# Kernel optimization log

Measured on AMD Instinct MI355X. Metric: run time of the kernel, lower is better.

## Reference

```python
import jax, jax.numpy as jnp
import numpy as np

H, W, K = 256, 256, 512
Z_THRESHOLD = 3.0
EPS = 1e-8


def setup_inputs() -> dict:
    key = jax.random.key(0)
    k1, k2, k3, k4 = jax.random.split(key, 4)
    # positions uniform in [0,H] x [0,W] x [0,64]
    positions = jax.random.uniform(k1, (K, 3)) * jnp.array([H, W, 64.0], jnp.float32)
    # scales: sigma_x, sigma_y in [1,5]; sigma_z in [0.5,2]
    s_xy = 1.0 + 4.0 * jax.random.uniform(k2, (K, 2))
    s_z = 0.5 + 1.5 * jax.random.uniform(k2, (K, 1))
    scales = jnp.concatenate([s_xy, s_z], axis=-1)
    opacity = jax.random.uniform(k3, (K,))
    intensity = jax.random.uniform(k4, (K,))
    z_target = jnp.array([32.0], jnp.float32)
    return {"positions": positions, "scales": scales, "opacity": opacity,
            "intensity": intensity, "z_target": z_target}


def reference(positions, scales, opacity, intensity, z_target):
    # z culling: instead of boolean gather (data-dependent shape), zero out
    # effective weights of culled Gaussians -> identical math (alpha=0 terms
    # contribute nothing and leave transmittance unchanged).
    z_dist = (z_target - positions[:, 2]) / (scales[:, 2] + EPS)          # (K,)
    z_mask = jnp.abs(z_dist) < Z_THRESHOLD
    z_weight = jnp.exp(-0.5 * z_dist ** 2)
    eff_w = jnp.where(z_mask, opacity * z_weight, 0.0)                    # (K,)

    grid_y = jnp.arange(H, dtype=positions.dtype)[:, None, None]         # (H,1,1)
    grid_x = jnp.arange(W, dtype=positions.dtype)[None, :, None]         # (1,W,1)
    # matches torch: dx pairs row-coord with mu_x, dy pairs col-coord with mu_y
    dxn = (grid_y - positions[:, 0]) / (scales[:, 0] + EPS)               # (H,W,K)
    dyn = (grid_x - positions[:, 1]) / (scales[:, 1] + EPS)               # (H,W,K)
    gauss = jnp.exp(-0.5 * (dxn ** 2 + dyn ** 2))                         # (H,W,K)

    # alpha compositing, sorted by weight descending
    alpha = jnp.clip(gauss * eff_w, 0.0, 0.99)
    order = jnp.argsort(-eff_w)
    alpha = alpha[:, :, order]
    s_int = intensity[order]
    trans = jnp.cumprod(1.0 - alpha, axis=-1)
    trans = jnp.concatenate([jnp.ones_like(trans[:, :, :1]), trans[:, :, :-1]], axis=-1)
    rendered = jnp.sum(trans * alpha * s_int, axis=-1)                    # (H,W)
    return rendered[None]                                                 # (1,H,W)
```

## Files before the change

### kernel.cpp

```cpp
#include <hip/hip_runtime.h>

#define IH 256
#define IW 256
#define NK 512
#define ZTH 3.0f
#define EPSV 1e-8f

__launch_bounds__(256, 4)
__global__ void slice_render_fused(const float* __restrict__ positions,
                                   const float* __restrict__ scales,
                                   const float* __restrict__ opacity,
                                   const float* __restrict__ intensity,
                                   const float* __restrict__ z_target,
                                   float* __restrict__ out) {
    __shared__ float s_pos[3 * NK];
    __shared__ float s_scl[3 * NK];
    __shared__ float s_opa[NK];
    __shared__ float s_int[NK];
    __shared__ float s_w[NK];
    __shared__ int   s_idx[NK];
    __shared__ float s_py[NK], s_isy[NK], s_rowfac[NK], s_it[NK];
    __shared__ int   s_cnt;

    const int tid = threadIdx.x;
    const float zt = z_target[0];

    for (int i = tid; i < 3 * NK; i += 256) {
        s_pos[i] = positions[i];
        s_scl[i] = scales[i];
    }
    for (int i = tid; i < NK; i += 256) {
        s_opa[i] = opacity[i];
        s_int[i] = intensity[i];
    }
    if (tid == 0) s_cnt = 0;
    __syncthreads();

    for (int k = tid; k < NK; k += 256) {
        float zd = (zt - s_pos[3 * k + 2]) / (s_scl[3 * k + 2] + EPSV);
        float w = 0.0f;
        if (fabsf(zd) < ZTH) w = s_opa[k] * __expf(-0.5f * zd * zd);
        if (w > 0.0f) {
            int p = atomicAdd(&s_cnt, 1);
            s_w[p] = w;
            s_idx[p] = k;
        }
    }
    __syncthreads();

    const int m = s_cnt;
    if (m == 0) { out[blockIdx.x * IW + tid] = 0.0f; return; }

    int msort = 2;
    while (msort < m) msort <<= 1;

    for (int k = m + tid; k < msort; k += 256) { s_w[k] = -1.0f; s_idx[k] = NK; }

    const int half = msort >> 1;
    for (int size = 2; size <= msort; size <<= 1) {
        for (int stride = size >> 1; stride > 0; stride >>= 1) {
            __syncthreads();
            for (int p = tid; p < half; p += 256) {
                int i = ((p & ~(stride - 1)) << 1) | (p & (stride - 1));
                int j = i | stride;
                bool desc = ((i & size) == 0);
                float wi = s_w[i], wj = s_w[j];
                int   ii = s_idx[i], ij = s_idx[j];
                bool cb_ji = (wj > wi) || (wj == wi && ij < ii);
                bool cb_ij = (wi > wj) || (wi == wj && ii < ij);
                if (desc ? cb_ji : cb_ij) {
                    s_w[i] = wj;  s_w[j] = wi;
                    s_idx[i] = ij; s_idx[j] = ii;
                }
            }
        }
    }
    __syncthreads();

    const float y = (float)blockIdx.x;
    for (int k = tid; k < m; k += 256) {
        int j = s_idx[k];
        float px  = s_pos[3 * j + 0];
        float isx = 1.0f / (s_scl[3 * j + 0] + EPSV);
        float dx  = (y - px) * isx;
        s_rowfac[k] = __expf(-0.5f * dx * dx) * s_w[k];
        s_py[k]   = s_pos[3 * j + 1];
        s_isy[k]  = 1.0f / (s_scl[3 * j + 1] + EPSV);
        s_it[k]   = s_int[j];
    }
    __syncthreads();

    const float x = (float)tid;
    float T = 1.0f;
    float acc = 0.0f;
    for (int k = 0; k < m; ++k) {
        float dy = (x - s_py[k]) * s_isy[k];
        float a  = fminf(__expf(-0.5f * dy * dy) * s_rowfac[k], 0.99f);
        acc += T * a * s_it[k];
        T   *= 1.0f - a;
        if (__all(T < 1e-6f)) break;
    }
    out[blockIdx.x * IW + tid] = acc;
}

extern "C" void kernel_launch(void* const* d_in, const int* in_sizes, int n_in,
                              void* d_out, int out_size, void* d_ws, size_t ws_size,
                              hipStream_t stream) {
    (void)in_sizes; (void)n_in; (void)out_size; (void)d_ws; (void)ws_size;
    const float* positions = (const float*)d_in[0];
    const float* scales    = (const float*)d_in[1];
    const float* opacity   = (const float*)d_in[2];
    const float* intensity = (const float*)d_in[3];
    const float* z_target  = (const float*)d_in[4];
    float* out = (float*)d_out;
    hipLaunchKernelGGL(slice_render_fused, dim3(IH), dim3(256), 0, stream,
                       positions, scales, opacity, intensity, z_target, out);
}
```

Baseline: 76.54 us.

## Replace bitonic sort with rank sort and pack per-gaussian data into float4

After: 69.65 us. 9.0% less time.

```diff
diff --git a/kernel.cpp b/kernel.cpp
--- a/kernel.cpp
+++ b/kernel.cpp
@@ -13,33 +13,21 @@
                                    const float* __restrict__ intensity,
                                    const float* __restrict__ z_target,
                                    float* __restrict__ out) {
-    __shared__ float s_pos[3 * NK];
-    __shared__ float s_scl[3 * NK];
-    __shared__ float s_opa[NK];
-    __shared__ float s_int[NK];
-    __shared__ float s_w[NK];
-    __shared__ int   s_idx[NK];
-    __shared__ float s_py[NK], s_isy[NK], s_rowfac[NK], s_it[NK];
-    __shared__ int   s_cnt;
+    __shared__ float  s_w[NK];
+    __shared__ int    s_idx[NK];
+    __shared__ float4 s_srt[NK + 8];
+    __shared__ int    s_cnt;
 
     const int tid = threadIdx.x;
     const float zt = z_target[0];
 
-    for (int i = tid; i < 3 * NK; i += 256) {
-        s_pos[i] = positions[i];
-        s_scl[i] = scales[i];
-    }
-    for (int i = tid; i < NK; i += 256) {
-        s_opa[i] = opacity[i];
-        s_int[i] = intensity[i];
-    }
     if (tid == 0) s_cnt = 0;
     __syncthreads();
 
     for (int k = tid; k < NK; k += 256) {
-        float zd = (zt - s_pos[3 * k + 2]) / (s_scl[3 * k + 2] + EPSV);
+        float zd = (zt - positions[3 * k + 2]) / (scales[3 * k + 2] + EPSV);
         float w = 0.0f;
-        if (fabsf(zd) < ZTH) w = s_opa[k] * __expf(-0.5f * zd * zd);
+        if (fabsf(zd) < ZTH) w = opacity[k] * __expf(-0.5f * zd * zd);
         if (w > 0.0f) {
             int p = atomicAdd(&s_cnt, 1);
             s_w[p] = w;
@@ -48,56 +36,44 @@
     }
     __syncthreads();
 
-    const int m = s_cnt;
-    if (m == 0) { out[blockIdx.x * IW + tid] = 0.0f; return; }
+    const int m  = s_cnt;
+    const int mp = (m + 7) & ~7;
+    const float y = (float)blockIdx.x;
 
-    int msort = 2;
-    while (msort < m) msort <<= 1;
-
-    for (int k = m + tid; k < msort; k += 256) { s_w[k] = -1.0f; s_idx[k] = NK; }
-
-    const int half = msort >> 1;
-    for (int size = 2; size <= msort; size <<= 1) {
-        for (int stride = size >> 1; stride > 0; stride >>= 1) {
-            __syncthreads();
-            for (int p = tid; p < half; p += 256) {
-                int i = ((p & ~(stride - 1)) << 1) | (p & (stride - 1));
-                int j = i | stride;
-                bool desc = ((i & size) == 0);
-                float wi = s_w[i], wj = s_w[j];
-                int   ii = s_idx[i], ij = s_idx[j];
-                bool cb_ji = (wj > wi) || (wj == wi && ij < ii);
-                bool cb_ij = (wi > wj) || (wi == wj && ii < ij);
-                if (desc ? cb_ji : cb_ij) {
-                    s_w[i] = wj;  s_w[j] = wi;
-                    s_idx[i] = ij; s_idx[j] = ii;
-                }
+    for (int i = tid; i < mp; i += 256) {
+        if (i < m) {
+            float wi = s_w[i];
+            int   ji = s_idx[i];
+            int rank = 0;
+            for (int j = 0; j < m; ++j) {
+                float wj = s_w[j];
+                int   jj = s_idx[j];
+                rank += (wj > wi || (wj == wi && jj < ji)) ? 1 : 0;
             }
+            float px  = positions[3 * ji + 0];
+            float py  = positions[3 * ji + 1];
+            float isx = 1.0f / (scales[3 * ji + 0] + EPSV);
+            float isy = 1.0f / (scales[3 * ji + 1] + EPSV);
+            float dx  = (y - px) * isx;
+            float rowfac = __expf(-0.5f * dx * dx) * wi;
+            s_srt[rank] = make_float4(py, isy, rowfac, intensity[ji]);
+        } else {
+            s_srt[i] = make_float4(0.0f, 1.0f, 0.0f, 0.0f);
         }
     }
     __syncthreads();
 
-    const float y = (float)blockIdx.x;
-    for (int k = tid; k < m; k += 256) {
-        int j = s_idx[k];
-        float px  = s_pos[3 * j + 0];
-        float isx = 1.0f / (s_scl[3 * j + 0] + EPSV);
-        float dx  = (y - px) * isx;
-        s_rowfac[k] = __expf(-0.5f * dx * dx) * s_w[k];
-        s_py[k]   = s_pos[3 * j + 1];
-        s_isy[k]  = 1.0f / (s_scl[3 * j + 1] + EPSV);
-        s_it[k]   = s_int[j];
-    }
-    __syncthreads();
-
     const float x = (float)tid;
-    float T = 1.0f;
-    float acc = 0.0f;
-    for (int k = 0; k < m; ++k) {
-        float dy = (x - s_py[k]) * s_isy[k];
-        float a  = fminf(__expf(-0.5f * dy * dy) * s_rowfac[k], 0.99f);
-        acc += T * a * s_it[k];
-        T   *= 1.0f - a;
+    float T = 1.0f, acc = 0.0f;
+    for (int k0 = 0; k0 < mp; k0 += 8) {
+#pragma unroll
+        for (int u = 0; u < 8; ++u) {
+            float4 g = s_srt[k0 + u];
+            float dy = (x - g.x) * g.y;
+            float a  = fminf(__expf(-0.5f * dy * dy) * g.z, 0.99f);
+            acc += T * a * g.w;
+            T   *= 1.0f - a;
+        }
         if (__all(T < 1e-6f)) break;
     }
     out[blockIdx.x * IW + tid] = acc;
```
